# Kernel optimization log

Measured on AMD Instinct MI355X. Metric: run time of the kernel, lower is better.

## Reference

```python
import jax, jax.numpy as jnp
import numpy as np

N_EMBD = 4096
N_HEAD = 2
HEAD_DIM = N_EMBD // N_HEAD  # 2048; note seq_len T must equal HEAD_DIM for the bias broadcast
B, T = 8, HEAD_DIM


def setup_inputs() -> dict:
    key = jax.random.key(0)
    ks = jax.random.split(key, 6)
    s = 1.0 / np.sqrt(N_EMBD)
    return {
        "x": jax.random.normal(ks[0], (B, T, N_EMBD), dtype=jnp.float32),
        "Wq": jax.random.normal(ks[1], (N_EMBD, N_EMBD), dtype=jnp.float32) * s,
        "Wk": jax.random.normal(ks[2], (N_EMBD, N_EMBD), dtype=jnp.float32) * s,
        "Wv": jax.random.normal(ks[3], (N_EMBD, N_EMBD), dtype=jnp.float32) * s,
        "Wo": jax.random.normal(ks[4], (N_EMBD, N_EMBD), dtype=jnp.float32) * s,
        "position_bias": jax.random.normal(ks[5], (N_HEAD, HEAD_DIM), dtype=jnp.float32) * 0.02,
    }


def reference(x, Wq, Wk, Wv, Wo, position_bias):
    Bb, Tt, C = x.shape
    H, D = N_HEAD, C // N_HEAD
    # nn.Linear(bias=False): y = x @ W.T
    q = (x @ Wq.T).reshape(Bb, Tt, H, D).transpose(0, 2, 1, 3)  # (B,H,T,D)
    k = (x @ Wk.T).reshape(Bb, Tt, H, D).transpose(0, 2, 1, 3)
    v = (x @ Wv.T).reshape(Bb, Tt, H, D).transpose(0, 2, 1, 3)
    scale = 1.0 / jnp.sqrt(jnp.asarray(D, dtype=x.dtype))
    scores = jnp.einsum("bhtd,bhsd->bhts", q, k) * scale  # (B,H,T,T)
    # position_bias (H,D) -> (1,H,1,D); broadcasts over key axis since D == T
    scores = scores + position_bias[None, :, None, :]
    atten = jax.nn.softmax(scores, axis=-1)  # mask=None, dropout=0.0 -> identity
    y = jnp.einsum("bhts,bhsd->bhtd", atten, v)  # (B,H,T,D)
    y = y.transpose(0, 2, 1, 3).reshape(Bb, Tt, C)
    y = y @ Wo.T
    return (y, atten)
```

## Files before the change

kernel.cpp:

```cpp
#include <hip/hip_runtime.h>
#include <hip/hip_bf16.h>
#include <cstdint>
#include <cstddef>


typedef short short8_t __attribute__((ext_vector_type(8)));
typedef float f32x4   __attribute__((ext_vector_type(4)));

__device__ __forceinline__ short f2bf(float f) {
  unsigned u = __builtin_bit_cast(unsigned, f);
  u = (u + 0x7FFFu + ((u >> 16) & 1u)) >> 16;
  return (short)u;
}

__device__ __forceinline__ short8_t cvt8(f32x4 a, f32x4 b) {
  short8_t r;
  r[0] = f2bf(a[0]); r[1] = f2bf(a[1]); r[2] = f2bf(a[2]); r[3] = f2bf(a[3]);
  r[4] = f2bf(b[0]); r[5] = f2bf(b[1]); r[6] = f2bf(b[2]); r[7] = f2bf(b[3]);
  return r;
}

__device__ __forceinline__ void gld_lds16(const void* g, void* l) {
  __builtin_amdgcn_global_load_lds(
      (const __attribute__((address_space(1))) void*)g,
      (__attribute__((address_space(3))) void*)l, 16, 0, 0);
}

__global__ __launch_bounds__(256)
void cvt_f32_bf16(const float* __restrict__ src, short* __restrict__ dst, int n8) {
  for (int i = blockIdx.x * blockDim.x + threadIdx.x; i < n8;
       i += gridDim.x * blockDim.x) {
    const f32x4* p = (const f32x4*)(src + (size_t)i * 8);
    f32x4 a = __builtin_nontemporal_load(p);
    f32x4 b = __builtin_nontemporal_load(p + 1);
    *(short8_t*)(dst + (size_t)i * 8) = cvt8(a, b);
  }
}

__global__ __launch_bounds__(256)
void cvt3_f32_bf16(const float* __restrict__ s0, const float* __restrict__ s1,
                   const float* __restrict__ s2, short* __restrict__ dst,
                   int n8each) {
  const int total = 3 * n8each;
  for (int i = blockIdx.x * blockDim.x + threadIdx.x; i < total;
       i += gridDim.x * blockDim.x) {
    const int which = i / n8each;
    const int off   = i - which * n8each;
    const float* s  = (which == 0) ? s0 : (which == 1) ? s1 : s2;
    const f32x4* p = (const f32x4*)(s + (size_t)off * 8);
    f32x4 a = __builtin_nontemporal_load(p);
    f32x4 b = __builtin_nontemporal_load(p + 1);
    *(short8_t*)(dst + (size_t)i * 8) = cvt8(a, b);
  }
}

template<int MODE>
__global__ __launch_bounds__(512, 2)
void gemm256(const short* __restrict__ Ag, const short* __restrict__ Bg,
             void* __restrict__ Cg, const float* __restrict__ bias) {
  constexpr int K  = (MODE == 3 || MODE == 4) ? 2048 : 4096;
  constexpr int NS = K / 32;

  __shared__ short lds[65536];

  const int tid = threadIdx.x;

  const int bid = blockIdx.x;
  const int id  = (bid & 7) * (gridDim.x >> 3) + (bid >> 3);

  int m0, n0, z = 0;
  size_t aoff = 0, boff = 0;
  if constexpr (MODE == 3 || MODE == 4) {
    z  = id >> 6;
    m0 = ((id >> 3) & 7) << 8;
    n0 = (id & 7) << 8;
    aoff = boff = (size_t)z << 22;
  } else {
    m0 = (id >> 4) << 8;
    n0 = (id & 15) << 8;
  }

  const int r0 = tid >> 2;
  const int qs = ((tid & 3) ^ ((r0 >> 1) & 3)) << 3;
  const short* Ap0 = Ag + aoff + (size_t)(m0 + r0) * K + qs;
  const short* Ap1 = Ap0 + (size_t)128 * K;
  const short* Bp0 = Bg + boff + (size_t)(n0 + r0) * K + qs;
  const short* Bp1 = Bp0 + (size_t)128 * K;
  short* la0 = &lds[0]    + tid * 8;
  short* la1 = la0 + 4096;
  short* lb0 = &lds[8192] + tid * 8;
  short* lb1 = lb0 + 4096;

  auto STAGE = [&](int t) {
    const int s = (t & 3) * 16384;
    const int k = t * 32;
    gld_lds16(Ap0 + k, la0 + s);
    gld_lds16(Ap1 + k, la1 + s);
    gld_lds16(Bp0 + k, lb0 + s);
    gld_lds16(Bp1 + k, lb1 + s);
  };

  const int l  = tid & 63;
  const int fr = l & 15;
  const int kq = l >> 4;
  const int wm = (tid >> 8) << 7;
  const int wn = ((tid >> 6) & 3) << 6;
  const int slotP = (kq ^ ((fr >> 1) & 3)) << 3;
  const int aB = (wm + fr) * 32 + slotP;
  const int bB = 8192 + (wn + fr) * 32 + slotP;

  f32x4 acc[8][4] = {};
  short8_t fA[8], fB[4], gA[8], gB[4];

  auto phaseF = [&](int p, short8_t (&cA)[8], short8_t (&cB)[4],
                    short8_t (&nA)[8], short8_t (&nB)[4]) {
    asm volatile("s_waitcnt vmcnt(4)" ::: "memory");
    __builtin_amdgcn_s_barrier();
    STAGE(p + 3);
    const short* sl = &lds[((p + 1) & 3) * 16384];
    __builtin_amdgcn_s_setprio(1);
#pragma unroll
    for (int gq = 0; gq < 4; ++gq) {
      nA[2 * gq]     = *(const short8_t*)&sl[aB + (2 * gq) * 512];
      nA[2 * gq + 1] = *(const short8_t*)&sl[aB + (2 * gq + 1) * 512];
      nB[gq]         = *(const short8_t*)&sl[bB + gq * 512];
#pragma unroll
      for (int mm = 0; mm < 2; ++mm)
#pragma unroll
        for (int n = 0; n < 4; ++n)
          acc[2 * gq + mm][n] = __builtin_amdgcn_mfma_f32_16x16x32_bf16(
              cA[2 * gq + mm], cB[n], acc[2 * gq + mm][n], 0, 0, 0);
    }
#pragma unroll
    for (int u = 0; u < 12; ++u) {
      __builtin_amdgcn_sched_group_barrier(0x100, 1, 0);
      __builtin_amdgcn_sched_group_barrier(0x008, 2, 0);
    }
    __builtin_amdgcn_sched_group_barrier(0x008, 8, 0);
    __builtin_amdgcn_s_setprio(0);
  };

  auto phaseT = [&](int p, short8_t (&cA)[8], short8_t (&cB)[4],
                    short8_t (&nA)[8], short8_t (&nB)[4]) {
    if (p + 2 < NS) {
      asm volatile("s_waitcnt vmcnt(4)" ::: "memory");
    } else {
      asm volatile("s_waitcnt vmcnt(0)" ::: "memory");
    }
    __builtin_amdgcn_s_barrier();
    if (p + 3 < NS) STAGE(p + 3);
    if (p + 1 < NS) {
      const short* sl = &lds[((p + 1) & 3) * 16384];
#pragma unroll
      for (int m = 0; m < 8; ++m) nA[m] = *(const short8_t*)&sl[aB + m * 512];
#pragma unroll
      for (int n = 0; n < 4; ++n) nB[n] = *(const short8_t*)&sl[bB + n * 512];
    }
    __builtin_amdgcn_s_setprio(1);
#pragma unroll
    for (int m = 0; m < 8; ++m)
#pragma unroll
      for (int n = 0; n < 4; ++n)
        acc[m][n] = __builtin_amdgcn_mfma_f32_16x16x32_bf16(cA[m], cB[n], acc[m][n], 0, 0, 0);
    __builtin_amdgcn_s_setprio(0);
  };

  STAGE(0); STAGE(1); STAGE(2);
  asm volatile("s_waitcnt vmcnt(8)" ::: "memory");
  __builtin_amdgcn_s_barrier();
  {
    const short* sl = &lds[0];
#pragma unroll
    for (int m = 0; m < 8; ++m) fA[m] = *(const short8_t*)&sl[aB + m * 512];
#pragma unroll
    for (int n = 0; n < 4; ++n) fB[n] = *(const short8_t*)&sl[bB + n * 512];
  }

  int p = 0;
  for (; p < NS - 4; p += 2) {
    phaseF(p,     fA, fB, gA, gB);
    phaseF(p + 1, gA, gB, fA, fB);
  }
  phaseT(NS - 4, fA, fB, gA, gB);
  phaseT(NS - 3, gA, gB, fA, fB);
  phaseT(NS - 2, fA, fB, gA, gB);
  phaseT(NS - 1, gA, gB, fA, fB);

#pragma unroll
  for (int m = 0; m < 8; ++m) {
#pragma unroll
    for (int n = 0; n < 4; ++n) {
#pragma unroll
      for (int r = 0; r < 4; ++r) {
        const int gm = m0 + wm + m * 16 + kq * 4 + r;
        const int gn = n0 + wn + n * 16 + fr;
        const float v = acc[m][n][r];
        if constexpr (MODE == 0) {
          short* dst = (short*)Cg;
          const int bh = ((gm >> 11) << 1) + (gn >> 11);
          dst[((size_t)bh << 22) + ((size_t)(gm & 2047) << 11) + (gn & 2047)] = f2bf(v);
        } else if constexpr (MODE == 2) {
          short* dst = (short*)Cg;
          const int bh = ((gm >> 11) << 1) + (gn >> 11);
          dst[((size_t)bh << 22) + ((size_t)(gn & 2047) << 11) + (gm & 2047)] = f2bf(v);
        } else if constexpr (MODE == 3) {
          float* dst = (float*)Cg;
          const float sv = v * 0.022097086912079608f + bias[((z & 1) << 11) + gn];
          dst[((size_t)z << 22) + ((size_t)gm << 11) + gn] = sv;
        } else if constexpr (MODE == 4) {
          short* dst = (short*)Cg;
          const size_t row = ((size_t)(z >> 1) << 11) + gm;
          dst[(row << 12) + ((size_t)(z & 1) << 11) + gn] = f2bf(v);
        } else {
          float* dst = (float*)Cg;
          dst[(size_t)gm * 4096 + gn] = v;
        }
      }
    }
  }
}

__global__ __launch_bounds__(256)
void softmax_rows(float* __restrict__ attn, short* __restrict__ outb) {
  float* row  = attn + ((size_t)blockIdx.x << 11);
  short* rowb = outb + ((size_t)blockIdx.x << 11);
  const int tid = threadIdx.x;

  f32x4 v0 = *(const f32x4*)(row + tid * 8);
  f32x4 v1 = *(const f32x4*)(row + tid * 8 + 4);

  float m = fmaxf(fmaxf(fmaxf(v0[0], v0[1]), fmaxf(v0[2], v0[3])),
                  fmaxf(fmaxf(v1[0], v1[1]), fmaxf(v1[2], v1[3])));
#pragma unroll
  for (int off = 1; off < 64; off <<= 1) m = fmaxf(m, __shfl_xor(m, off));

  __shared__ float redm[4];
  __shared__ float reds[4];
  if ((tid & 63) == 0) redm[tid >> 6] = m;
  __syncthreads();
  m = fmaxf(fmaxf(redm[0], redm[1]), fmaxf(redm[2], redm[3]));

  float e[8];
#pragma unroll
  for (int i = 0; i < 4; ++i) e[i]     = expf(v0[i] - m);
#pragma unroll
  for (int i = 0; i < 4; ++i) e[4 + i] = expf(v1[i] - m);
  float s = 0.f;
#pragma unroll
  for (int i = 0; i < 8; ++i) s += e[i];
#pragma unroll
  for (int off = 1; off < 64; off <<= 1) s += __shfl_xor(s, off);
  if ((tid & 63) == 0) reds[tid >> 6] = s;
  __syncthreads();
  s = reds[0] + reds[1] + reds[2] + reds[3];

  const float inv = 1.0f / s;
  f32x4 o0, o1;
#pragma unroll
  for (int i = 0; i < 4; ++i) { o0[i] = e[i] * inv; o1[i] = e[4 + i] * inv; }
  *(f32x4*)(row + tid * 8)     = o0;
  *(f32x4*)(row + tid * 8 + 4) = o1;
  *(short8_t*)(rowb + tid * 8) = cvt8(o0, o1);
}

extern "C" void kernel_launch(void* const* d_in, const int* in_sizes, int n_in,
                              void* d_out, int out_size, void* d_ws, size_t ws_size,
                              hipStream_t stream) {
  const float* x  = (const float*)d_in[0];
  const float* Wq = (const float*)d_in[1];
  const float* Wk = (const float*)d_in[2];
  const float* Wv = (const float*)d_in[3];
  const float* Wo = (const float*)d_in[4];
  const float* pb = (const float*)d_in[5];

  float* y_out = (float*)d_out;
  float* attn  = y_out + (size_t)8 * 2048 * 4096;

  const size_t NEED = 4ull * 67108864ull * 2ull;
  if (ws_size < NEED) return;
  short* buf0 = (short*)d_ws;
  short* buf1 = buf0 + 67108864;
  short* buf2 = buf1 + 67108864;
  short* buf3 = buf2 + 67108864;

  short* xb      = buf0;
  short* qb      = buf1;
  short* kb      = buf2;
  short* vtb     = buf3;
  short* wob     = buf0;
  short* attn_bf = buf1;
  short* yb      = buf2;
  short* wqkv    = (short*)attn;

  const dim3 blk512(512);
  const dim3 blk(256);
  const dim3 gcv(2048);
  const dim3 g1k(1024);

  cvt_f32_bf16<<<gcv, blk, 0, stream>>>(x, xb, 67108864 / 8);
  cvt3_f32_bf16<<<gcv, blk, 0, stream>>>(Wq, Wk, Wv, wqkv, 16777216 / 8);

  gemm256<0><<<g1k, blk512, 0, stream>>>(xb, wqkv,                qb,  nullptr);
  gemm256<0><<<g1k, blk512, 0, stream>>>(xb, wqkv + 16777216,     kb,  nullptr);
  gemm256<2><<<g1k, blk512, 0, stream>>>(xb, wqkv + 2 * 16777216, vtb, nullptr);

  cvt_f32_bf16<<<gcv, blk, 0, stream>>>(Wo, wob, 16777216 / 8);

  gemm256<3><<<g1k, blk512, 0, stream>>>(qb, kb, attn, pb);
  softmax_rows<<<dim3(32768), blk, 0, stream>>>(attn, attn_bf);
  gemm256<4><<<g1k, blk512, 0, stream>>>(attn_bf, vtb, yb, nullptr);
  gemm256<5><<<g1k, blk512, 0, stream>>>(yb, wob, y_out, nullptr);
}
```

Before: 2.700 ms.

## Switch GEMM kernels from 256x256 to 128x128 tiles with 256-thread blocks

Replaces the 512-thread 256x256-tile GEMM with a 256-thread 128x128-tile version using a fragment-ordered LDS layout, and launches four times as many blocks. This gives more blocks for scheduling and a simpler LDS read pattern with half the shared memory per block. In exchange, each output element costs more global and L2 traffic because arithmetic intensity per tile is lower.

```diff
diff --git a/kernel.cpp b/kernel.cpp
--- a/kernel.cpp
+++ b/kernel.cpp
@@ -55,13 +55,13 @@
 }
 
 template<int MODE>
-__global__ __launch_bounds__(512, 2)
-void gemm256(const short* __restrict__ Ag, const short* __restrict__ Bg,
+__global__ __launch_bounds__(256, 2)
+void gemm128(const short* __restrict__ Ag, const short* __restrict__ Bg,
              void* __restrict__ Cg, const float* __restrict__ bias) {
   constexpr int K  = (MODE == 3 || MODE == 4) ? 2048 : 4096;
   constexpr int NS = K / 32;
 
-  __shared__ short lds[65536];
+  __shared__ short lds[32768];
 
   const int tid = threadIdx.x;
 
@@ -71,77 +71,71 @@
   int m0, n0, z = 0;
   size_t aoff = 0, boff = 0;
   if constexpr (MODE == 3 || MODE == 4) {
-    z  = id >> 6;
-    m0 = ((id >> 3) & 7) << 8;
-    n0 = (id & 7) << 8;
+    z  = id >> 8;
+    m0 = ((id >> 4) & 15) << 7;
+    n0 = (id & 15) << 7;
     aoff = boff = (size_t)z << 22;
   } else {
-    m0 = (id >> 4) << 8;
-    n0 = (id & 15) << 8;
-  }
-
-  const int r0 = tid >> 2;
-  const int qs = ((tid & 3) ^ ((r0 >> 1) & 3)) << 3;
-  const short* Ap0 = Ag + aoff + (size_t)(m0 + r0) * K + qs;
-  const short* Ap1 = Ap0 + (size_t)128 * K;
-  const short* Bp0 = Bg + boff + (size_t)(n0 + r0) * K + qs;
-  const short* Bp1 = Bp0 + (size_t)128 * K;
-  short* la0 = &lds[0]    + tid * 8;
-  short* la1 = la0 + 4096;
-  short* lb0 = &lds[8192] + tid * 8;
-  short* lb1 = lb0 + 4096;
+    m0 = (id >> 5) << 7;
+    n0 = (id & 31) << 7;
+  }
+
+  const int l = tid & 63;
+  const int w = tid >> 6;
+
+  const int srow = l & 15;
+  const int skol = (l >> 4) * 8;
+  const short* ApS0 = Ag + aoff + (size_t)(m0 + 16 * w + srow) * K + skol;
+  const short* ApS1 = ApS0 + (size_t)64 * K;
+  const short* BpS0 = Bg + boff + (size_t)(n0 + 16 * w + srow) * K + skol;
+  const short* BpS1 = BpS0 + (size_t)64 * K;
+  short* lA0 = &lds[w * 512 + l * 8];
+  short* lA1 = &lds[(4 + w) * 512 + l * 8];
+  short* lB0 = &lds[4096 + w * 512 + l * 8];
+  short* lB1 = &lds[4096 + (4 + w) * 512 + l * 8];
 
   auto STAGE = [&](int t) {
-    const int s = (t & 3) * 16384;
+    const int s = (t & 3) * 8192;
     const int k = t * 32;
-    gld_lds16(Ap0 + k, la0 + s);
-    gld_lds16(Ap1 + k, la1 + s);
-    gld_lds16(Bp0 + k, lb0 + s);
-    gld_lds16(Bp1 + k, lb1 + s);
+    gld_lds16(ApS0 + k, lA0 + s);
+    gld_lds16(ApS1 + k, lA1 + s);
+    gld_lds16(BpS0 + k, lB0 + s);
+    gld_lds16(BpS1 + k, lB1 + s);
   };
 
-  const int l  = tid & 63;
-  const int fr = l & 15;
-  const int kq = l >> 4;
-  const int wm = (tid >> 8) << 7;
-  const int wn = ((tid >> 6) & 3) << 6;
-  const int slotP = (kq ^ ((fr >> 1) & 3)) << 3;
-  const int aB = (wm + fr) * 32 + slotP;
-  const int bB = 8192 + (wn + fr) * 32 + slotP;
-
-  f32x4 acc[8][4] = {};
-  short8_t fA[8], fB[4], gA[8], gB[4];
-
-  auto phaseF = [&](int p, short8_t (&cA)[8], short8_t (&cB)[4],
-                    short8_t (&nA)[8], short8_t (&nB)[4]) {
+  const int aU = (w >> 1) * 4;
+  const int bU = (w & 1) * 4;
+  const int l8 = l * 8;
+
+  f32x4 acc[4][4] = {};
+  short8_t fA[4], fB[4], gA[4], gB[4];
+
+  auto phaseF = [&](int p, short8_t (&cA)[4], short8_t (&cB)[4],
+                    short8_t (&nA)[4], short8_t (&nB)[4]) {
     asm volatile("s_waitcnt vmcnt(4)" ::: "memory");
     __builtin_amdgcn_s_barrier();
     STAGE(p + 3);
-    const short* sl = &lds[((p + 1) & 3) * 16384];
+    const short* sl = &lds[((p + 1) & 3) * 8192];
     __builtin_amdgcn_s_setprio(1);
 #pragma unroll
-    for (int gq = 0; gq < 4; ++gq) {
-      nA[2 * gq]     = *(const short8_t*)&sl[aB + (2 * gq) * 512];
-      nA[2 * gq + 1] = *(const short8_t*)&sl[aB + (2 * gq + 1) * 512];
-      nB[gq]         = *(const short8_t*)&sl[bB + gq * 512];
-#pragma unroll
-      for (int mm = 0; mm < 2; ++mm)
-#pragma unroll
-        for (int n = 0; n < 4; ++n)
-          acc[2 * gq + mm][n] = __builtin_amdgcn_mfma_f32_16x16x32_bf16(
-              cA[2 * gq + mm], cB[n], acc[2 * gq + mm][n], 0, 0, 0);
-    }
-#pragma unroll
-    for (int u = 0; u < 12; ++u) {
+    for (int i = 0; i < 4; ++i) {
+      nA[i] = *(const short8_t*)&sl[(aU + i) * 512 + l8];
+      nB[i] = *(const short8_t*)&sl[4096 + (bU + i) * 512 + l8];
+#pragma unroll
+      for (int n = 0; n < 4; ++n)
+        acc[i][n] = __builtin_amdgcn_mfma_f32_16x16x32_bf16(
+            cA[i], cB[n], acc[i][n], 0, 0, 0);
+    }
+#pragma unroll
+    for (int u = 0; u < 8; ++u) {
       __builtin_amdgcn_sched_group_barrier(0x100, 1, 0);
       __builtin_amdgcn_sched_group_barrier(0x008, 2, 0);
     }
-    __builtin_amdgcn_sched_group_barrier(0x008, 8, 0);
     __builtin_amdgcn_s_setprio(0);
   };
 
-  auto phaseT = [&](int p, short8_t (&cA)[8], short8_t (&cB)[4],
-                    short8_t (&nA)[8], short8_t (&nB)[4]) {
+  auto phaseT = [&](int p, short8_t (&cA)[4], short8_t (&cB)[4],
+                    short8_t (&nA)[4], short8_t (&nB)[4]) {
     if (p + 2 < NS) {
       asm volatile("s_waitcnt vmcnt(4)" ::: "memory");
     } else {
@@ -150,18 +144,20 @@
     __builtin_amdgcn_s_barrier();
     if (p + 3 < NS) STAGE(p + 3);
     if (p + 1 < NS) {
-      const short* sl = &lds[((p + 1) & 3) * 16384];
-#pragma unroll
-      for (int m = 0; m < 8; ++m) nA[m] = *(const short8_t*)&sl[aB + m * 512];
-#pragma unroll
-      for (int n = 0; n < 4; ++n) nB[n] = *(const short8_t*)&sl[bB + n * 512];
+      const short* sl = &lds[((p + 1) & 3) * 8192];
+#pragma unroll
+      for (int i = 0; i < 4; ++i) {
+        nA[i] = *(const short8_t*)&sl[(aU + i) * 512 + l8];
+        nB[i] = *(const short8_t*)&sl[4096 + (bU + i) * 512 + l8];
+      }
     }
     __builtin_amdgcn_s_setprio(1);
 #pragma unroll
-    for (int m = 0; m < 8; ++m)
+    for (int i = 0; i < 4; ++i)
 #pragma unroll
       for (int n = 0; n < 4; ++n)
-        acc[m][n] = __builtin_amdgcn_mfma_f32_16x16x32_bf16(cA[m], cB[n], acc[m][n], 0, 0, 0);
+        acc[i][n] = __builtin_amdgcn_mfma_f32_16x16x32_bf16(
+            cA[i], cB[n], acc[i][n], 0, 0, 0);
     __builtin_amdgcn_s_setprio(0);
   };
 
@@ -171,9 +167,10 @@
   {
     const short* sl = &lds[0];
 #pragma unroll
-    for (int m = 0; m < 8; ++m) fA[m] = *(const short8_t*)&sl[aB + m * 512];
-#pragma unroll
-    for (int n = 0; n < 4; ++n) fB[n] = *(const short8_t*)&sl[bB + n * 512];
+    for (int i = 0; i < 4; ++i) {
+      fA[i] = *(const short8_t*)&sl[(aU + i) * 512 + l8];
+      fB[i] = *(const short8_t*)&sl[4096 + (bU + i) * 512 + l8];
+    }
   }
 
   int p = 0;
@@ -186,8 +183,12 @@
   phaseT(NS - 2, fA, fB, gA, gB);
   phaseT(NS - 1, gA, gB, fA, fB);
 
-#pragma unroll
-  for (int m = 0; m < 8; ++m) {
+  const int fr = l & 15;
+  const int kq = l >> 4;
+  const int wm = (w >> 1) << 6;
+  const int wn = (w & 1) << 6;
+#pragma unroll
+  for (int m = 0; m < 4; ++m) {
 #pragma unroll
     for (int n = 0; n < 4; ++n) {
 #pragma unroll
@@ -292,22 +293,21 @@
   short* yb      = buf2;
   short* wqkv    = (short*)attn;
 
-  const dim3 blk512(512);
   const dim3 blk(256);
   const dim3 gcv(2048);
-  const dim3 g1k(1024);
+  const dim3 g4k(4096);
 
   cvt_f32_bf16<<<gcv, blk, 0, stream>>>(x, xb, 67108864 / 8);
   cvt3_f32_bf16<<<gcv, blk, 0, stream>>>(Wq, Wk, Wv, wqkv, 16777216 / 8);
 
-  gemm256<0><<<g1k, blk512, 0, stream>>>(xb, wqkv,                qb,  nullptr);
-  gemm256<0><<<g1k, blk512, 0, stream>>>(xb, wqkv + 16777216,     kb,  nullptr);
-  gemm256<2><<<g1k, blk512, 0, stream>>>(xb, wqkv + 2 * 16777216, vtb, nullptr);
+  gemm128<0><<<g4k, blk, 0, stream>>>(xb, wqkv,                qb,  nullptr);
+  gemm128<0><<<g4k, blk, 0, stream>>>(xb, wqkv + 16777216,     kb,  nullptr);
+  gemm128<2><<<g4k, blk, 0, stream>>>(xb, wqkv + 2 * 16777216, vtb, nullptr);
 
   cvt_f32_bf16<<<gcv, blk, 0, stream>>>(Wo, wob, 16777216 / 8);
 
-  gemm256<3><<<g1k, blk512, 0, stream>>>(qb, kb, attn, pb);
+  gemm128<3><<<g4k, blk, 0, stream>>>(qb, kb, attn, pb);
   softmax_rows<<<dim3(32768), blk, 0, stream>>>(attn, attn_bf);
-  gemm256<4><<<g1k, blk512, 0, stream>>>(attn_bf, vtb, yb, nullptr);
-  gemm256<5><<<g1k, blk512, 0, stream>>>(yb, wob, y_out, nullptr);
-}
+  gemm128<4><<<g4k, blk, 0, stream>>>(attn_bf, vtb, yb, nullptr);
+  gemm128<5><<<g4k, blk, 0, stream>>>(yb, wob, y_out, nullptr);
+}
```

New measurement: 5.329 ms. 97.3% more time.
